# Performance work log

Measured on AMD Instinct MI355X. Metric: run time of the kernel, lower is better.

## Reference

```python
import jax, jax.numpy as jnp
import numpy as np

B, C, IMG, P = 64, 3, 224, 16
HP = IMG // P                 # 14 patches per side
N = HP * HP                   # 196 patches
R = 196                       # num_superpixels
D, HEADS, DEPTH = 384, 6, 12
HD = D // HEADS
MLP = 4 * D
CLS = 1000
WIN = 4                       # local attention window radius
SEQ = R + 1


def setup_inputs() -> dict:
    key = jax.random.key(0)
    ks = jax.random.split(key, 16)
    nrm = lambda k, s: jax.random.normal(k, s, jnp.float32) * 0.02
    return dict(
        x=jax.random.normal(ks[0], (B, C, IMG, IMG), jnp.float32),
        seg=jax.random.randint(ks[1], (B, IMG, IMG), 0, R, jnp.int32),
        patch_W=nrm(ks[2], (C * P * P, D)), patch_b=jnp.zeros((D,), jnp.float32),
        cls_token=nrm(ks[3], (1, 1, D)),
        pos_W=nrm(ks[4], (2, D)), pos_b=jnp.zeros((D,), jnp.float32),
        cls_pos=nrm(ks[5], (D,)),
        ln1_w=jnp.ones((DEPTH, D), jnp.float32), ln1_b=jnp.zeros((DEPTH, D), jnp.float32),
        qkv_W=nrm(ks[6], (DEPTH, D, 3 * D)), qkv_b=jnp.zeros((DEPTH, 3 * D), jnp.float32),
        proj_W=nrm(ks[7], (DEPTH, D, D)), proj_b=jnp.zeros((DEPTH, D), jnp.float32),
        ln2_w=jnp.ones((DEPTH, D), jnp.float32), ln2_b=jnp.zeros((DEPTH, D), jnp.float32),
        mlp_W1=nrm(ks[8], (DEPTH, D, MLP)), mlp_b1=jnp.zeros((DEPTH, MLP), jnp.float32),
        mlp_W2=nrm(ks[9], (DEPTH, MLP, D)), mlp_b2=jnp.zeros((DEPTH, D), jnp.float32),
        norm_w=jnp.ones((D,), jnp.float32), norm_b=jnp.zeros((D,), jnp.float32),
        head_W=nrm(ks[10], (D, CLS)), head_b=jnp.zeros((CLS,), jnp.float32),
    )


def _ln(x, w, b):
    m = x.mean(-1, keepdims=True)
    v = ((x - m) ** 2).mean(-1, keepdims=True)
    return (x - m) * jax.lax.rsqrt(v + 1e-5) * w + b


def _forward(x, seg, patch_W, patch_b, cls_token, pos_W, pos_b, cls_pos,
             ln1_w, ln1_b, qkv_W, qkv_b, proj_W, proj_b, ln2_w, ln2_b,
             mlp_W1, mlp_b1, mlp_W2, mlp_b2, norm_w, norm_b, head_W, head_b):
    # --- patch embedding (conv stride==kernel == patchify + matmul) -> [B,N,D]
    xp = x.reshape(B, C, HP, P, HP, P).transpose(0, 2, 4, 1, 3, 5).reshape(B, N, C * P * P)
    emb = xp @ patch_W + patch_b
    # --- patch -> superpixel id: segmentation label at patch center pixel
    centers = jnp.arange(HP) * P + P // 2
    patch_seg = seg[:, centers[:, None], centers[None, :]].reshape(B, N)
    # --- mean pooling per superpixel (fused segment reduce over all batches)
    pids = (jnp.arange(B, dtype=patch_seg.dtype)[:, None] * R + patch_seg).reshape(-1)
    sums = jax.ops.segment_sum(emb.reshape(-1, D), pids, num_segments=B * R)
    cnts = jax.ops.segment_sum(jnp.ones((B * N,), emb.dtype), pids, num_segments=B * R)
    pooled = (sums / jnp.maximum(cnts, 1.0)[:, None]).reshape(B, R, D)
    # --- superpixel centroids via pixel-level segment reduce -> [B,R,2] (x,y)
    coords = jnp.arange(IMG, dtype=jnp.float32) / IMG
    yg, xg = jnp.meshgrid(coords, coords, indexing='ij')
    gid = (jnp.arange(B, dtype=seg.dtype)[:, None] * R + seg.reshape(B, -1)).reshape(-1)
    pix = IMG * IMG
    pcnt = jax.ops.segment_sum(jnp.ones((B * pix,), jnp.float32), gid, num_segments=B * R)
    ysum = jax.ops.segment_sum(jnp.broadcast_to(yg.reshape(-1), (B, pix)).reshape(-1), gid, num_segments=B * R)
    xsum = jax.ops.segment_sum(jnp.broadcast_to(xg.reshape(-1), (B, pix)).reshape(-1), gid, num_segments=B * R)
    safe = jnp.maximum(pcnt, 1.0)
    cx = jnp.where(pcnt > 0, xsum / safe, 0.5)
    cy = jnp.where(pcnt > 0, ysum / safe, 0.5)
    centroids = jnp.stack([cx, cy], axis=-1).reshape(B, R, 2)
    # --- prepend cls token, add dynamic (centroid-based) positional encoding
    tok = jnp.concatenate([jnp.broadcast_to(cls_token, (B, 1, D)), pooled], axis=1)
    pos = jnp.concatenate([jnp.broadcast_to(cls_pos[None, None, :], (B, 1, D)),
                           centroids @ pos_W + pos_b], axis=1)
    h = tok + pos
    # --- local (banded) attention mask; cls token attends globally
    idx = jnp.arange(SEQ)
    band = jnp.abs(idx[:, None] - idx[None, :]) <= WIN
    band = band | (idx[:, None] == 0) | (idx[None, :] == 0)
    neg = jnp.float32(-1e9)
    scale = 1.0 / np.sqrt(HD)
    for l in range(DEPTH):
        z = _ln(h, ln1_w[l], ln1_b[l])
        qkv = (z @ qkv_W[l] + qkv_b[l]).reshape(B, SEQ, 3, HEADS, HD)
        q, k, v = qkv[:, :, 0], qkv[:, :, 1], qkv[:, :, 2]
        s = jnp.einsum('bqhd,bkhd->bhqk', q, k) * scale
        s = jnp.where(band[None, None], s, neg)
        a = jax.nn.softmax(s, axis=-1)
        o = jnp.einsum('bhqk,bkhd->bqhd', a, v).reshape(B, SEQ, D)
        h = h + o @ proj_W[l] + proj_b[l]
        z = _ln(h, ln2_w[l], ln2_b[l])
        h = h + jax.nn.gelu(z @ mlp_W1[l] + mlp_b1[l]) @ mlp_W2[l] + mlp_b2[l]
    h = _ln(h, norm_w, norm_b)
    return h[:, 0] @ head_W + head_b


def reference(x, seg, patch_W, patch_b, cls_token, pos_W, pos_b, cls_pos,
              ln1_w, ln1_b, qkv_W, qkv_b, proj_W, proj_b, ln2_w, ln2_b,
              mlp_W1, mlp_b1, mlp_W2, mlp_b2, norm_w, norm_b, head_W, head_b):
    return _forward(x, seg, patch_W, patch_b, cls_token, pos_W, pos_b, cls_pos,
                    ln1_w, ln1_b, qkv_W, qkv_b, proj_W, proj_b, ln2_w, ln2_b,
                    mlp_W1, mlp_b1, mlp_W2, mlp_b2, norm_w, norm_b, head_W, head_b)
```

## Files before the change

### kernel.cpp

```cpp
#include <hip/hip_runtime.h>
#include <hip/hip_bf16.h>
#include <math.h>

typedef unsigned short ushort_t;
typedef unsigned int uint_t;
typedef __attribute__((ext_vector_type(8))) short short8;
typedef __attribute__((ext_vector_type(4))) float f32x4;

#define BATCH 64
#define CHN 3
#define IMG 224
#define PATCH 16
#define HP 14
#define NPATCH 196
#define RSEG 196
#define DMODEL 384
#define HEADS 6
#define HD 64
#define DEPTH 12
#define MLPD 1536
#define CLS 1000
#define WIN 4
#define SEQ 197
#define PIX (IMG*IMG)
#define PATCHK (CHN*PATCH*PATCH)
#define CPARTS 16
#define PPP (PIX / CPARTS)

__device__ __forceinline__ ushort_t f2bf(float f) {
  uint_t u = __float_as_uint(f);
  u += 0x7FFFu + ((u >> 16) & 1u);
  return (ushort_t)(u >> 16);
}
__device__ __forceinline__ float bf2f(ushort_t u) {
  return __uint_as_float((uint_t)u << 16);
}
__device__ __forceinline__ float gelu_tanh(float x) {
  float z = 0.7978845608028654f * (x + 0.044715f * x * x * x);
  z = fminf(fmaxf(z, -15.f), 15.f);
  float t = exp2f(2.8853900817779268f * z);
  return x * t / (t + 1.f);
}
__device__ __forceinline__ int xcd_swizzle(int bid, int nwg) {
  int q = nwg >> 3, r = nwg & 7;
  int xcd = bid & 7, idx = bid >> 3;
  int start = (xcd < r) ? xcd * (q + 1) : r * (q + 1) + (xcd - r) * q;
  return start + idx;
}
__device__ __forceinline__ float dot16bf(const ushort_t* a, const ushort_t* b) {
  const uint_t* a32 = (const uint_t*)a;
  const uint_t* b32 = (const uint_t*)b;
  float acc = 0.f;
#pragma unroll
  for (int w = 0; w < 8; w++) {
    uint_t ka = a32[w], kb = b32[w];
    acc += bf2f((ushort_t)(ka & 0xffff)) * bf2f((ushort_t)(kb & 0xffff));
    acc += bf2f((ushort_t)(ka >> 16)) * bf2f((ushort_t)(kb >> 16));
  }
  return acc;
}

__global__ __launch_bounds__(256) void convtrans_kernel(
    const float* __restrict__ W, ushort_t* __restrict__ Wt, int K, int N) {
  __shared__ float t[32][33];
  int k0 = blockIdx.y * 32, n0 = blockIdx.x * 32;
  const float* Wl = W + (size_t)blockIdx.z * K * N;
  ushort_t* Wtl = Wt + (size_t)blockIdx.z * K * N;
  int tx = threadIdx.x & 31, ty = threadIdx.x >> 5;
#pragma unroll
  for (int i = 0; i < 32; i += 8)
    t[ty + i][tx] = Wl[(size_t)(k0 + ty + i) * N + n0 + tx];
  __syncthreads();
#pragma unroll
  for (int i = 0; i < 32; i += 8)
    Wtl[(size_t)(n0 + ty + i) * K + k0 + tx] = f2bf(t[tx][ty + i]);
}

__global__ __launch_bounds__(256) void patchify_kernel(
    const float* __restrict__ x, ushort_t* __restrict__ xp, int total) {
  int idx = blockIdx.x * 256 + threadIdx.x;
  if (idx >= total) return;
  int k = idx % PATCHK;
  int m = idx / PATCHK;
  int n = m % NPATCH;
  int b = m / NPATCH;
  int hi = n / HP, wi = n % HP;
  int c = k / (PATCH * PATCH);
  int rem = k % (PATCH * PATCH);
  int pi = rem / PATCH, pj = rem % PATCH;
  int row = hi * PATCH + pi, col = wi * PATCH + pj;
  xp[idx] = f2bf(x[(((size_t)b * CHN + c) * IMG + row) * IMG + col]);
}

template <int BMT, bool GELU, bool RESID, int OUTMODE>
__global__ __launch_bounds__(256) void gemm_gl(
    const ushort_t* __restrict__ A, const ushort_t* __restrict__ Bt,
    const float* __restrict__ bias, const float* __restrict__ resid,
    void* __restrict__ Cout, int M, int N, int K, int gx) {
  constexpr int AWS = BMT * 2;
  constexpr int AI = AWS / 64;
  constexpr int MF = 4;
  constexpr int NF = (BMT == 128) ? 4 : 2;
  constexpr int BUF_U = (BMT + 128) * 64;
  constexpr int CS_U = BMT * 136;
  constexpr int SMEM_U = (2 * BUF_U > CS_U) ? 2 * BUF_U : CS_U;
  __shared__ __align__(16) ushort_t smem[SMEM_U];
  int tid = threadIdx.x;
  int wave = tid >> 6, lane = tid & 63;
  int flat = xcd_swizzle(blockIdx.x, gridDim.x);
  int bx = flat % gx, by = flat / gx;
  int bm = by * BMT, bn = bx * 128;
  int wr = (BMT == 128) ? (wave >> 1) * 64 : 0;
  int wc = (BMT == 128) ? (wave & 1) * 64 : wave * 32;
  f32x4 acc[MF][NF];
#pragma unroll
  for (int m = 0; m < MF; m++)
#pragma unroll
    for (int n = 0; n < NF; n++)
#pragma unroll
      for (int e = 0; e < 4; e++) acc[m][n][e] = 0.f;

  int r = lane & 15;
  int cfrag = lane >> 4;

  auto STAGE = [&](int buf, int k0) {
    ushort_t* As = smem + buf * BUF_U;
    ushort_t* Bs = As + BMT * 64;
#pragma unroll
    for (int j = 0; j < AI; j++) {
      int s = wave * AWS + j * 64 + lane;
      int row = s >> 3;
      int cp = s & 7;
      int c = cp ^ ((row >> 1) & 7);
      const ushort_t* src = A + (size_t)(bm + row) * K + k0 + c * 8;
      ushort_t* dst = As + (size_t)(wave * AWS + j * 64) * 8;
      __builtin_amdgcn_global_load_lds(
          (const __attribute__((address_space(1))) void*)src,
          (__attribute__((address_space(3))) void*)dst, 16, 0, 0);
    }
#pragma unroll
    for (int j = 0; j < 4; j++) {
      int s = wave * 256 + j * 64 + lane;
      int row = s >> 3;
      int cp = s & 7;
      int c = cp ^ ((row >> 1) & 7);
      const ushort_t* src = Bt + (size_t)(bn + row) * K + k0 + c * 8;
      ushort_t* dst = Bs + (size_t)(wave * 256 + j * 64) * 8;
      __builtin_amdgcn_global_load_lds(
          (const __attribute__((address_space(1))) void*)src,
          (__attribute__((address_space(3))) void*)dst, 16, 0, 0);
    }
  };

  STAGE(0, 0);
  __syncthreads();
  int cur = 0;
  for (int k0 = 0; k0 < K; k0 += 64) {
    if (k0 + 64 < K) STAGE(cur ^ 1, k0 + 64);
    ushort_t* As = smem + cur * BUF_U;
    ushort_t* Bs = As + BMT * 64;
#pragma unroll
    for (int kk = 0; kk < 2; kk++) {
      short8 af[MF], bfr[NF];
#pragma unroll
      for (int m = 0; m < MF; m++) {
        int row = wr + m * 16 + r;
        int sl = (kk * 4 + cfrag) ^ ((row >> 1) & 7);
        af[m] = *(const short8*)(As + row * 64 + sl * 8);
      }
#pragma unroll
      for (int n = 0; n < NF; n++) {
        int row = wc + n * 16 + r;
        int sl = (kk * 4 + cfrag) ^ ((row >> 1) & 7);
        bfr[n] = *(const short8*)(Bs + row * 64 + sl * 8);
      }
#pragma unroll
      for (int m = 0; m < MF; m++)
#pragma unroll
        for (int n = 0; n < NF; n++)
          acc[m][n] = __builtin_amdgcn_mfma_f32_16x16x32_bf16(
              af[m], bfr[n], acc[m][n], 0, 0, 0);
    }
    __syncthreads();
    cur ^= 1;
  }
  int q4 = (lane >> 4) * 4;
  if (OUTMODE == 0) {
#pragma unroll
    for (int n = 0; n < NF; n++) {
      int col = bn + wc + n * 16 + r;
      float bi = bias[col];
#pragma unroll
      for (int m = 0; m < MF; m++) {
#pragma unroll
        for (int e = 0; e < 4; e++) {
          int row = bm + wr + m * 16 + q4 + e;
          if (row < M) {
            float v = acc[m][n][e] + bi;
            if (GELU) v = gelu_tanh(v);
            if (RESID) v += resid[(size_t)row * N + col];
            ((float*)Cout)[(size_t)row * N + col] = v;
          }
        }
      }
    }
  } else {
    ushort_t* Cs = smem;
#pragma unroll
    for (int n = 0; n < NF; n++) {
      int lc = wc + n * 16 + r;
      float bi = bias[bn + lc];
#pragma unroll
      for (int m = 0; m < MF; m++) {
#pragma unroll
        for (int e = 0; e < 4; e++) {
          int lr = wr + m * 16 + q4 + e;
          float v = acc[m][n][e] + bi;
          if (GELU) v = gelu_tanh(v);
          if (RESID) v += resid[(size_t)(bm + lr) * N + bn + lc];
          Cs[lr * 136 + lc] = f2bf(v);
        }
      }
    }
    __syncthreads();
    constexpr int CHUNKS = BMT * 16;
#pragma unroll
    for (int c = 0; c < CHUNKS / 256; c++) {
      int id = c * 256 + tid;
      int row = id >> 4, ch = id & 15;
      int grow = bm + row;
      if (grow < M) {
        short8 val = *(const short8*)(Cs + row * 136 + ch * 8);
        int gcol = bn + ch * 8;
        if (OUTMODE == 1) {
          *(short8*)((ushort_t*)Cout + (size_t)grow * N + gcol) = val;
        } else {
          int b_ = grow / SEQ, t_ = grow - b_ * SEQ;
          int which = gcol / DMODEL;
          int hcol = gcol - which * DMODEL;
          int hh = hcol >> 6, d0 = hcol & 63;
          *(short8*)((ushort_t*)Cout +
                     ((((size_t)b_ * 3 + which) * HEADS + hh) * SEQ + t_) * 64 +
                     d0) = val;
        }
      }
    }
  }
}

__global__ __launch_bounds__(256) void zeroacc_kernel(int* __restrict__ g,
                                                      int n) {
  int i = blockIdx.x * 256 + threadIdx.x;
  if (i < n) g[i] = 0;
}

__global__ __launch_bounds__(256) void centroid_part_kernel(
    const int* __restrict__ seg, int* __restrict__ gacc) {
  __shared__ int cnt[RSEG], si[RSEG], sj[RSEG];
  int b = blockIdx.x, part = blockIdx.y, tid = threadIdx.x;
  for (int r = tid; r < RSEG; r += 256) { cnt[r] = 0; si[r] = 0; sj[r] = 0; }
  __syncthreads();
  const int* s = seg + (size_t)b * PIX;
  int p0 = part * PPP;
  for (int p = p0 + tid; p < p0 + PPP; p += 256) {
    int r = s[p];
    int i = p / IMG, j = p % IMG;
    atomicAdd(&cnt[r], 1);
    atomicAdd(&si[r], i);
    atomicAdd(&sj[r], j);
  }
  __syncthreads();
  for (int r = tid; r < RSEG; r += 256) {
    int c = cnt[r];
    if (c | si[r] | sj[r]) {
      int* g = gacc + ((size_t)b * RSEG + r) * 3;
      atomicAdd(&g[0], c);
      atomicAdd(&g[1], si[r]);
      atomicAdd(&g[2], sj[r]);
    }
  }
}
__global__ __launch_bounds__(256) void centroid_fin_kernel(
    const int* __restrict__ gacc, float* __restrict__ cent) {
  int b = blockIdx.x, tid = threadIdx.x;
  for (int r = tid; r < RSEG; r += 256) {
    const int* g = gacc + ((size_t)b * RSEG + r) * 3;
    int c = g[0];
    float cx = 0.5f, cy = 0.5f;
    if (c > 0) {
      cx = ((float)g[2] / (float)IMG) / (float)c;
      cy = ((float)g[1] / (float)IMG) / (float)c;
    }
    cent[((size_t)b * RSEG + r) * 2 + 0] = cx;
    cent[((size_t)b * RSEG + r) * 2 + 1] = cy;
  }
}

__global__ __launch_bounds__(256) void patchseg_kernel(
    const int* __restrict__ seg, int* __restrict__ pseg) {
  int idx = blockIdx.x * 256 + threadIdx.x;
  if (idx >= BATCH * NPATCH) return;
  int n = idx % NPATCH, b = idx / NPATCH;
  int hi = n / HP, wi = n % HP;
  pseg[idx] = seg[(size_t)b * PIX + (8 + hi * PATCH) * IMG + (8 + wi * PATCH)];
}

__global__ __launch_bounds__(64) void buildlists_kernel(
    const int* __restrict__ pseg, int* __restrict__ starts,
    int* __restrict__ lists) {
  __shared__ int cnt[RSEG];
  int b = blockIdx.x;
  if (threadIdx.x != 0) return;
  const int* ps = pseg + b * NPATCH;
  for (int r = 0; r < RSEG; r++) cnt[r] = 0;
  for (int n = 0; n < NPATCH; n++) cnt[ps[n]]++;
  int run = 0;
  int* st = starts + b * (RSEG + 1);
  for (int r = 0; r < RSEG; r++) {
    st[r] = run;
    int c = cnt[r];
    cnt[r] = run;
    run += c;
  }
  st[RSEG] = run;
  int* li = lists + b * NPATCH;
  for (int n = 0; n < NPATCH; n++) {
    int r = ps[n];
    li[cnt[r]++] = n;
  }
}

__global__ __launch_bounds__(384) void pool_assemble_kernel(
    const float* __restrict__ emb, const float* __restrict__ cent,
    const int* __restrict__ starts, const int* __restrict__ lists,
    const float* __restrict__ cls_token, const float* __restrict__ cls_pos,
    const float* __restrict__ pos_W, const float* __restrict__ pos_b,
    float* __restrict__ h) {
  int t = blockIdx.x;
  int b = t / SEQ, s = t % SEQ;
  int d = threadIdx.x;
  float out;
  if (s == 0) {
    out = cls_token[d] + cls_pos[d];
  } else {
    int r = s - 1;
    int st = starts[b * (RSEG + 1) + r];
    int en = starts[b * (RSEG + 1) + r + 1];
    float acc = 0.f;
    for (int i = st; i < en; i++) {
      int n = lists[b * NPATCH + i];
      acc += emb[((size_t)b * NPATCH + n) * DMODEL + d];
    }
    int cnt = en - st;
    float pooled = acc / (float)(cnt > 0 ? cnt : 1);
    float cx = cent[((size_t)b * RSEG + r) * 2 + 0];
    float cy = cent[((size_t)b * RSEG + r) * 2 + 1];
    out = pooled + cx * pos_W[d] + cy * pos_W[DMODEL + d] + pos_b[d];
  }
  h[(size_t)t * DMODEL + d] = out;
}

template <bool OUTBF16>
__global__ __launch_bounds__(128) void ln_kernel(
    const float* __restrict__ in, void* __restrict__ out,
    const float* __restrict__ w, const float* __restrict__ b, int inStride) {
  int row = blockIdx.x;
  const float* xr = in + (size_t)row * inStride;
  int tid = threadIdx.x;
  float x0 = xr[tid], x1 = xr[tid + 128], x2 = xr[tid + 256];
  float s = x0 + x1 + x2;
  float s2 = x0 * x0 + x1 * x1 + x2 * x2;
#pragma unroll
  for (int off = 32; off; off >>= 1) {
    s += __shfl_xor(s, off);
    s2 += __shfl_xor(s2, off);
  }
  __shared__ float ls[2], ls2[2];
  int wv = tid >> 6;
  if ((tid & 63) == 0) { ls[wv] = s; ls2[wv] = s2; }
  __syncthreads();
  float S = ls[0] + ls[1], S2 = ls2[0] + ls2[1];
  float m = S / (float)DMODEL;
  float var = S2 / (float)DMODEL - m * m;
  float rs = rsqrtf(var + 1e-5f);
#pragma unroll
  for (int i = 0; i < 3; i++) {
    int dd = tid + i * 128;
    float xv = (i == 0) ? x0 : (i == 1) ? x1 : x2;
    float v = (xv - m) * rs * w[dd] + b[dd];
    if (OUTBF16)
      ((ushort_t*)out)[(size_t)row * DMODEL + dd] = f2bf(v);
    else
      ((float*)out)[(size_t)row * DMODEL + dd] = v;
  }
}

__global__ __launch_bounds__(256) void attn_kernel(
    const ushort_t* __restrict__ qkvp, ushort_t* __restrict__ o) {
  int wave = threadIdx.x >> 6, lane = threadIdx.x & 63;
  int gi = blockIdx.x * 4 + wave;
  int hh = blockIdx.y, b = blockIdx.z;
  const size_t hstride = (size_t)HEADS * SEQ * 64;
  size_t base0 = ((size_t)b * 3 * HEADS + hh) * SEQ * 64;
  const ushort_t* Qh = qkvp + base0;
  const ushort_t* Kh = qkvp + base0 + hstride;
  const ushort_t* Vh = qkvp + base0 + 2 * hstride;
  if (gi < 49) {
    int q0 = 1 + gi * 4;
    int base = q0 - 4;
    if (base < 1) base = 1;
    int row = lane >> 2, dq = lane & 3;
    int key = (row == 0) ? 0 : base + row - 1;
    bool rowvalid = (key <= 196);
    int kaddr = rowvalid ? key : 196;
    const uint_t* kp = (const uint_t*)(Kh + (size_t)kaddr * 64 + dq * 16);
    uint_t kf[8];
#pragma unroll
    for (int w = 0; w < 8; w++) kf[w] = kp[w];
    float v[16];
#pragma unroll
    for (int r = 0; r < 16; r++) {
      int kr = (r == 0) ? 0 : base + r - 1;
      if (kr > 196) kr = 196;
      v[r] = bf2f(Vh[(size_t)kr * 64 + lane]);
    }
#pragma unroll
    for (int i = 0; i < 4; i++) {
      int qi = q0 + i;
      const uint_t* qp = (const uint_t*)(Qh + (size_t)qi * 64 + dq * 16);
      float part = 0.f;
#pragma unroll
      for (int w = 0; w < 8; w++) {
        uint_t ka = kf[w], qa = qp[w];
        part += bf2f((ushort_t)(ka & 0xffff)) * bf2f((ushort_t)(qa & 0xffff));
        part += bf2f((ushort_t)(ka >> 16)) * bf2f((ushort_t)(qa >> 16));
      }
      part += __shfl_xor(part, 1);
      part += __shfl_xor(part, 2);
      int lo = qi - WIN;
      if (lo < 1) lo = 1;
      int hi = qi + WIN;
      if (hi > 196) hi = 196;
      bool valid = rowvalid && ((key == 0) || (key >= lo && key <= hi));
      float s = valid ? part * 0.125f : -1e30f;
      float mx = s;
      mx = fmaxf(mx, __shfl_xor(mx, 4));
      mx = fmaxf(mx, __shfl_xor(mx, 8));
      mx = fmaxf(mx, __shfl_xor(mx, 16));
      mx = fmaxf(mx, __shfl_xor(mx, 32));
      float p = valid ? expf(s - mx) : 0.f;
      float sum = p;
      sum += __shfl_xor(sum, 4);
      sum += __shfl_xor(sum, 8);
      sum += __shfl_xor(sum, 16);
      sum += __shfl_xor(sum, 32);
      float acc = 0.f;
#pragma unroll
      for (int r = 0; r < 16; r++) acc += __shfl(p, r * 4) * v[r];
      o[((size_t)(b * SEQ + qi)) * DMODEL + hh * HD + lane] = f2bf(acc / sum);
    }
  } else if (gi == 49) {
    const ushort_t* qr = Qh;
    float sc0 = -1e30f, sc1 = -1e30f, sc2 = -1e30f, sc3 = -1e30f;
#pragma unroll
    for (int c = 0; c < 4; c++) {
      int key = c * 64 + lane;
      float s = -1e30f;
      if (key < SEQ) {
        const ushort_t* kr = Kh + (size_t)key * 64;
        float acc = dot16bf(kr, qr) + dot16bf(kr + 16, qr + 16) +
                    dot16bf(kr + 32, qr + 32) + dot16bf(kr + 48, qr + 48);
        s = acc * 0.125f;
      }
      if (c == 0) sc0 = s; else if (c == 1) sc1 = s; else if (c == 2) sc2 = s; else sc3 = s;
    }
    float mx = fmaxf(fmaxf(sc0, sc1), fmaxf(sc2, sc3));
#pragma unroll
    for (int off = 32; off; off >>= 1) mx = fmaxf(mx, __shfl_xor(mx, off));
    float p0 = expf(sc0 - mx), p1 = expf(sc1 - mx);
    float p2 = expf(sc2 - mx), p3 = expf(sc3 - mx);
    float sum = p0 + p1 + p2 + p3;
#pragma unroll
    for (int off = 32; off; off >>= 1) sum += __shfl_xor(sum, off);
    float acc = 0.f;
#pragma unroll
    for (int c = 0; c < 4; c++) {
      float pc = (c == 0) ? p0 : (c == 1) ? p1 : (c == 2) ? p2 : p3;
      int jmax = (c < 3) ? 64 : (SEQ - 192);
      for (int jj = 0; jj < jmax; ++jj) {
        float pt = __shfl(pc, jj);
        acc += pt * bf2f(Vh[(size_t)(c * 64 + jj) * 64 + lane]);
      }
    }
    o[((size_t)(b * SEQ)) * DMODEL + hh * HD + lane] = f2bf(acc / sum);
  }
}

__global__ __launch_bounds__(256) void head_kernel(
    const float* __restrict__ hn, const float* __restrict__ W,
    const float* __restrict__ bias, float* __restrict__ out) {
  __shared__ float hs[DMODEL];
  int b = blockIdx.y;
  int c = blockIdx.x * 256 + threadIdx.x;
  for (int d = threadIdx.x; d < DMODEL; d += 256)
    hs[d] = hn[(size_t)b * DMODEL + d];
  __syncthreads();
  if (c >= CLS) return;
  float acc = bias[c];
  for (int d = 0; d < DMODEL; d++) acc += hs[d] * W[(size_t)d * CLS + c];
  out[(size_t)b * CLS + c] = acc;
}

extern "C" void kernel_launch(void* const* d_in, const int* in_sizes, int n_in,
                              void* d_out, int out_size, void* d_ws,
                              size_t ws_size, hipStream_t stream) {
  const float* x = (const float*)d_in[0];
  const int* seg = (const int*)d_in[1];
  const float* patch_W = (const float*)d_in[2];
  const float* patch_b = (const float*)d_in[3];
  const float* cls_token = (const float*)d_in[4];
  const float* pos_W = (const float*)d_in[5];
  const float* pos_b = (const float*)d_in[6];
  const float* cls_pos = (const float*)d_in[7];
  const float* ln1_w = (const float*)d_in[8];
  const float* ln1_b = (const float*)d_in[9];
  const float* qkv_W = (const float*)d_in[10];
  const float* qkv_b = (const float*)d_in[11];
  const float* proj_W = (const float*)d_in[12];
  const float* proj_b = (const float*)d_in[13];
  const float* ln2_w = (const float*)d_in[14];
  const float* ln2_b = (const float*)d_in[15];
  const float* mlp_W1 = (const float*)d_in[16];
  const float* mlp_b1 = (const float*)d_in[17];
  const float* mlp_W2 = (const float*)d_in[18];
  const float* mlp_b2 = (const float*)d_in[19];
  const float* norm_w = (const float*)d_in[20];
  const float* norm_b = (const float*)d_in[21];
  const float* head_W = (const float*)d_in[22];
  const float* head_b = (const float*)d_in[23];
  float* out = (float*)d_out;

  const int M0 = BATCH * NPATCH;
  const int MT = BATCH * SEQ;

  char* ws = (char*)d_ws;
  size_t off = 0;
  auto alloc = [&](size_t bytes) { char* p = ws + off; off += (bytes + 255) & ~(size_t)255; return p; };
  ushort_t* patch_Wt = (ushort_t*)alloc((size_t)PATCHK * DMODEL * 2);
  ushort_t* qkv_Wt   = (ushort_t*)alloc((size_t)DEPTH * DMODEL * 3 * DMODEL * 2);
  ushort_t* proj_Wt  = (ushort_t*)alloc((size_t)DEPTH * DMODEL * DMODEL * 2);
  ushort_t* mlp1_Wt  = (ushort_t*)alloc((size_t)DEPTH * DMODEL * MLPD * 2);
  ushort_t* mlp2_Wt  = (ushort_t*)alloc((size_t)DEPTH * MLPD * DMODEL * 2);
  char* big = alloc((size_t)MT * MLPD * 2);
  ushort_t* xp_bf = (ushort_t*)big;
  ushort_t* mlph_bf = (ushort_t*)big;
  ushort_t* qkvb = (ushort_t*)alloc((size_t)MT * 3 * DMODEL * 2);
  char* eo = alloc((size_t)M0 * DMODEL * 4);
  float* emb = (float*)eo;
  ushort_t* attno = (ushort_t*)eo;
  float* h = (float*)alloc((size_t)MT * DMODEL * 4);
  ushort_t* z_bf = (ushort_t*)alloc((size_t)MT * DMODEL * 2);
  float* cent = (float*)alloc((size_t)BATCH * RSEG * 2 * 4);
  float* hn = (float*)alloc((size_t)BATCH * DMODEL * 4);
  int* pseg = (int*)alloc((size_t)BATCH * NPATCH * 4);
  int* starts = (int*)alloc((size_t)BATCH * (RSEG + 1) * 4);
  int* lists = (int*)alloc((size_t)BATCH * NPATCH * 4);
  int* gacc = (int*)alloc((size_t)BATCH * RSEG * 3 * 4);

  convtrans_kernel<<<dim3(DMODEL / 32, PATCHK / 32, 1), 256, 0, stream>>>(
      patch_W, patch_Wt, PATCHK, DMODEL);
  convtrans_kernel<<<dim3(3 * DMODEL / 32, DMODEL / 32, DEPTH), 256, 0, stream>>>(
      qkv_W, qkv_Wt, DMODEL, 3 * DMODEL);
  convtrans_kernel<<<dim3(DMODEL / 32, DMODEL / 32, DEPTH), 256, 0, stream>>>(
      proj_W, proj_Wt, DMODEL, DMODEL);
  convtrans_kernel<<<dim3(MLPD / 32, DMODEL / 32, DEPTH), 256, 0, stream>>>(
      mlp_W1, mlp1_Wt, DMODEL, MLPD);
  convtrans_kernel<<<dim3(DMODEL / 32, MLPD / 32, DEPTH), 256, 0, stream>>>(
      mlp_W2, mlp2_Wt, MLPD, DMODEL);

  {
    int total = M0 * PATCHK;
    patchify_kernel<<<(total + 255) / 256, 256, 0, stream>>>(x, xp_bf, total);
  }
  gemm_gl<64, false, false, 0><<<(DMODEL / 128) * (M0 / 64), 256, 0, stream>>>(
      xp_bf, patch_Wt, patch_b, nullptr, emb, M0, DMODEL, PATCHK, DMODEL / 128);
  {
    int n = BATCH * RSEG * 3;
    zeroacc_kernel<<<(n + 255) / 256, 256, 0, stream>>>(gacc, n);
  }
  centroid_part_kernel<<<dim3(BATCH, CPARTS), 256, 0, stream>>>(seg, gacc);
  centroid_fin_kernel<<<BATCH, 256, 0, stream>>>(gacc, cent);
  patchseg_kernel<<<(M0 + 255) / 256, 256, 0, stream>>>(seg, pseg);
  buildlists_kernel<<<BATCH, 64, 0, stream>>>(pseg, starts, lists);
  pool_assemble_kernel<<<MT, 384, 0, stream>>>(emb, cent, starts, lists,
                                               cls_token, cls_pos, pos_W,
                                               pos_b, h);

  int gy128 = (MT + 127) / 128;
  int gy64 = MT / 64;
  for (int l = 0; l < DEPTH; l++) {
    ln_kernel<true><<<MT, 128, 0, stream>>>(h, z_bf, ln1_w + l * DMODEL,
                                            ln1_b + l * DMODEL, DMODEL);
    gemm_gl<128, false, false, 2><<<(3 * DMODEL / 128) * gy128, 256, 0, stream>>>(
        z_bf, qkv_Wt + (size_t)l * DMODEL * 3 * DMODEL, qkv_b + l * 3 * DMODEL,
        nullptr, qkvb, MT, 3 * DMODEL, DMODEL, 3 * DMODEL / 128);
    attn_kernel<<<dim3(13, HEADS, BATCH), 256, 0, stream>>>(qkvb, attno);
    gemm_gl<64, false, true, 0><<<(DMODEL / 128) * gy64, 256, 0, stream>>>(
        attno, proj_Wt + (size_t)l * DMODEL * DMODEL, proj_b + l * DMODEL, h,
        h, MT, DMODEL, DMODEL, DMODEL / 128);
    ln_kernel<true><<<MT, 128, 0, stream>>>(h, z_bf, ln2_w + l * DMODEL,
                                            ln2_b + l * DMODEL, DMODEL);
    gemm_gl<128, true, false, 1><<<(MLPD / 128) * gy128, 256, 0, stream>>>(
        z_bf, mlp1_Wt + (size_t)l * DMODEL * MLPD, mlp_b1 + l * MLPD, nullptr,
        mlph_bf, MT, MLPD, DMODEL, MLPD / 128);
    gemm_gl<64, false, true, 0><<<(DMODEL / 128) * gy64, 256, 0, stream>>>(
        mlph_bf, mlp2_Wt + (size_t)l * MLPD * DMODEL, mlp_b2 + l * DMODEL, h,
        h, MT, DMODEL, MLPD, DMODEL / 128);
  }
  ln_kernel<false><<<BATCH, 128, 0, stream>>>(h, hn, norm_w, norm_b,
                                              SEQ * DMODEL);
  head_kernel<<<dim3((CLS + 255) / 256, BATCH), 256, 0, stream>>>(
      hn, head_W, head_b, out);
}
```

Measured before the change: 1.927 ms.

## Vectorize patchify and layernorm, use one wave per LN row, raise MFMA priority

Patchify now has each thread load four consecutive floats and write four packed bf16 values. LayerNorm is rewritten so each wavefront handles one row with float2 loads and packed stores, which removes the shared-memory reduction and block barrier. The GEMM inner loop wraps its MFMA burst in s_setprio so waves doing math are favoured over those issuing loads. The LN grid relies on MT being divisible by 4 (MT = 64*197 = 12608, which is), and BATCH is also divisible by 4.

```diff
diff --git a/kernel.cpp b/kernel.cpp
--- a/kernel.cpp
+++ b/kernel.cpp
@@ -77,19 +77,25 @@
 }
 
 __global__ __launch_bounds__(256) void patchify_kernel(
-    const float* __restrict__ x, ushort_t* __restrict__ xp, int total) {
+    const float* __restrict__ x, ushort_t* __restrict__ xp, int total4) {
   int idx = blockIdx.x * 256 + threadIdx.x;
-  if (idx >= total) return;
-  int k = idx % PATCHK;
-  int m = idx / PATCHK;
+  if (idx >= total4) return;
+  int kq = idx % (PATCHK / 4);
+  int m = idx / (PATCHK / 4);
   int n = m % NPATCH;
   int b = m / NPATCH;
   int hi = n / HP, wi = n % HP;
-  int c = k / (PATCH * PATCH);
-  int rem = k % (PATCH * PATCH);
-  int pi = rem / PATCH, pj = rem % PATCH;
+  int k = kq * 4;
+  int c = k >> 8;
+  int rem = k & 255;
+  int pi = rem >> 4, pj = rem & 15;
   int row = hi * PATCH + pi, col = wi * PATCH + pj;
-  xp[idx] = f2bf(x[(((size_t)b * CHN + c) * IMG + row) * IMG + col]);
+  f32x4 v = *(const f32x4*)&x[(((size_t)b * CHN + c) * IMG + row) * IMG + col];
+  uint_t p0 = (uint_t)f2bf(v[0]) | ((uint_t)f2bf(v[1]) << 16);
+  uint_t p1 = (uint_t)f2bf(v[2]) | ((uint_t)f2bf(v[3]) << 16);
+  uint_t* dst = (uint_t*)(xp + (size_t)idx * 4);
+  dst[0] = p0;
+  dst[1] = p1;
 }
 
 template <int BMT, bool GELU, bool RESID, int OUTMODE>
@@ -174,12 +180,14 @@
         int sl = (kk * 4 + cfrag) ^ ((row >> 1) & 7);
         bfr[n] = *(const short8*)(Bs + row * 64 + sl * 8);
       }
+      __builtin_amdgcn_s_setprio(1);
 #pragma unroll
       for (int m = 0; m < MF; m++)
 #pragma unroll
         for (int n = 0; n < NF; n++)
           acc[m][n] = __builtin_amdgcn_mfma_f32_16x16x32_bf16(
               af[m], bfr[n], acc[m][n], 0, 0, 0);
+      __builtin_amdgcn_s_setprio(0);
     }
     __syncthreads();
     cur ^= 1;
@@ -361,37 +369,40 @@
 }
 
 template <bool OUTBF16>
-__global__ __launch_bounds__(128) void ln_kernel(
+__global__ __launch_bounds__(256) void ln_kernel(
     const float* __restrict__ in, void* __restrict__ out,
     const float* __restrict__ w, const float* __restrict__ b, int inStride) {
-  int row = blockIdx.x;
+  int wave = threadIdx.x >> 6, lane = threadIdx.x & 63;
+  int row = blockIdx.x * 4 + wave;
   const float* xr = in + (size_t)row * inStride;
-  int tid = threadIdx.x;
-  float x0 = xr[tid], x1 = xr[tid + 128], x2 = xr[tid + 256];
-  float s = x0 + x1 + x2;
-  float s2 = x0 * x0 + x1 * x1 + x2 * x2;
+  float2 v0 = *(const float2*)(xr + lane * 2);
+  float2 v1 = *(const float2*)(xr + 128 + lane * 2);
+  float2 v2 = *(const float2*)(xr + 256 + lane * 2);
+  float s = v0.x + v0.y + v1.x + v1.y + v2.x + v2.y;
+  float s2 = v0.x * v0.x + v0.y * v0.y + v1.x * v1.x + v1.y * v1.y +
+             v2.x * v2.x + v2.y * v2.y;
 #pragma unroll
   for (int off = 32; off; off >>= 1) {
     s += __shfl_xor(s, off);
     s2 += __shfl_xor(s2, off);
   }
-  __shared__ float ls[2], ls2[2];
-  int wv = tid >> 6;
-  if ((tid & 63) == 0) { ls[wv] = s; ls2[wv] = s2; }
-  __syncthreads();
-  float S = ls[0] + ls[1], S2 = ls2[0] + ls2[1];
-  float m = S / (float)DMODEL;
-  float var = S2 / (float)DMODEL - m * m;
+  float m = s / (float)DMODEL;
+  float var = s2 / (float)DMODEL - m * m;
   float rs = rsqrtf(var + 1e-5f);
 #pragma unroll
   for (int i = 0; i < 3; i++) {
-    int dd = tid + i * 128;
-    float xv = (i == 0) ? x0 : (i == 1) ? x1 : x2;
-    float v = (xv - m) * rs * w[dd] + b[dd];
-    if (OUTBF16)
-      ((ushort_t*)out)[(size_t)row * DMODEL + dd] = f2bf(v);
-    else
-      ((float*)out)[(size_t)row * DMODEL + dd] = v;
+    int d0 = i * 128 + lane * 2;
+    float x0 = (i == 0) ? v0.x : (i == 1) ? v1.x : v2.x;
+    float x1 = (i == 0) ? v0.y : (i == 1) ? v1.y : v2.y;
+    float o0 = (x0 - m) * rs * w[d0] + b[d0];
+    float o1 = (x1 - m) * rs * w[d0 + 1] + b[d0 + 1];
+    if (OUTBF16) {
+      uint_t pack = (uint_t)f2bf(o0) | ((uint_t)f2bf(o1) << 16);
+      *(uint_t*)((ushort_t*)out + (size_t)row * DMODEL + d0) = pack;
+    } else {
+      float2 pk = {o0, o1};
+      *(float2*)((float*)out + (size_t)row * DMODEL + d0) = pk;
+    }
   }
 }
 
@@ -579,8 +590,8 @@
       mlp_W2, mlp2_Wt, MLPD, DMODEL);
 
   {
-    int total = M0 * PATCHK;
-    patchify_kernel<<<(total + 255) / 256, 256, 0, stream>>>(x, xp_bf, total);
+    int total4 = M0 * PATCHK / 4;
+    patchify_kernel<<<(total4 + 255) / 256, 256, 0, stream>>>(x, xp_bf, total4);
   }
   gemm_gl<64, false, false, 0><<<(DMODEL / 128) * (M0 / 64), 256, 0, stream>>>(
       xp_bf, patch_Wt, patch_b, nullptr, emb, M0, DMODEL, PATCHK, DMODEL / 128);
@@ -599,8 +610,8 @@
   int gy128 = (MT + 127) / 128;
   int gy64 = MT / 64;
   for (int l = 0; l < DEPTH; l++) {
-    ln_kernel<true><<<MT, 128, 0, stream>>>(h, z_bf, ln1_w + l * DMODEL,
-                                            ln1_b + l * DMODEL, DMODEL);
+    ln_kernel<true><<<MT / 4, 256, 0, stream>>>(h, z_bf, ln1_w + l * DMODEL,
+                                                ln1_b + l * DMODEL, DMODEL);
     gemm_gl<128, false, false, 2><<<(3 * DMODEL / 128) * gy128, 256, 0, stream>>>(
         z_bf, qkv_Wt + (size_t)l * DMODEL * 3 * DMODEL, qkv_b + l * 3 * DMODEL,
         nullptr, qkvb, MT, 3 * DMODEL, DMODEL, 3 * DMODEL / 128);
@@ -608,8 +619,8 @@
     gemm_gl<64, false, true, 0><<<(DMODEL / 128) * gy64, 256, 0, stream>>>(
         attno, proj_Wt + (size_t)l * DMODEL * DMODEL, proj_b + l * DMODEL, h,
         h, MT, DMODEL, DMODEL, DMODEL / 128);
-    ln_kernel<true><<<MT, 128, 0, stream>>>(h, z_bf, ln2_w + l * DMODEL,
-                                            ln2_b + l * DMODEL, DMODEL);
+    ln_kernel<true><<<MT / 4, 256, 0, stream>>>(h, z_bf, ln2_w + l * DMODEL,
+                                                ln2_b + l * DMODEL, DMODEL);
     gemm_gl<128, true, false, 1><<<(MLPD / 128) * gy128, 256, 0, stream>>>(
         z_bf, mlp1_Wt + (size_t)l * DMODEL * MLPD, mlp_b1 + l * MLPD, nullptr,
         mlph_bf, MT, MLPD, DMODEL, MLPD / 128);
@@ -617,8 +628,8 @@
         mlph_bf, mlp2_Wt + (size_t)l * MLPD * DMODEL, mlp_b2 + l * DMODEL, h,
         h, MT, DMODEL, MLPD, DMODEL / 128);
   }
-  ln_kernel<false><<<BATCH, 128, 0, stream>>>(h, hn, norm_w, norm_b,
-                                              SEQ * DMODEL);
+  ln_kernel<false><<<BATCH / 4, 256, 0, stream>>>(h, hn, norm_w, norm_b,
+                                                  SEQ * DMODEL);
   head_kernel<<<dim3((CLS + 255) / 256, BATCH), 256, 0, stream>>>(
       hn, head_W, head_b, out);
 }
```

New measurement: 1.926 ms. Within noise of the previous version (-0.1%).
